# Kernel tuning notes

Hardware: AMD Instinct MI355X
Metric: run time of the kernel (lower is better)

The kernel has to match this reference:

```python
import jax, jax.numpy as jnp
import numpy as np

B = 64        # number of jagged segments
LMAX = 1024   # max_seq_len
D = 512       # input feature dim
K = 512       # output feature dim
NW = 128      # number of selectable weight matrices
T = 32768     # total jagged tokens (avg len 512)


def setup_inputs() -> dict:
    rng = np.random.default_rng(0)
    # Monotone offsets with avg segment length T//B = 512, jittered +/-200
    # so every length stays in (0, LMAX].
    offsets = np.arange(B + 1, dtype=np.int64) * (T // B)
    offsets[1:-1] += rng.integers(-200, 200, size=B - 1)
    key = jax.random.key(0)
    k1, k2, k3, k4 = jax.random.split(key, 4)
    jagged = jax.random.normal(k1, (T, D), dtype=jnp.float32)
    weight = jax.random.normal(k2, (NW, D, K), dtype=jnp.float32) * 0.02
    bias = jax.random.normal(k3, (NW, K), dtype=jnp.float32)
    index = jax.random.randint(k4, (B,), 0, NW)
    return {
        "max_seq_len": LMAX,
        "offsets": jnp.asarray(offsets),
        "index": index,
        "jagged": jagged,
        "weight": weight,
        "bias": bias,
    }


def reference(max_seq_len, offsets, index, jagged, weight, bias):
    # out[offsets[b]:offsets[b+1]] = jagged[offsets[b]:offsets[b+1]] @ weight[index[b]] + bias[index[b]]
    T_, Dd = jagged.shape
    Kk = weight.shape[-1]
    starts = offsets[:-1]            # [B]
    ends = offsets[1:]               # [B]
    pos = starts[:, None] + jnp.arange(max_seq_len)[None, :]   # [B, L] global row ids
    valid = pos < ends[:, None]                                # [B, L]
    safe = jnp.where(valid, pos, 0)
    padded = jnp.where(valid[..., None], jagged[safe], 0)      # [B, L, D]
    w = weight[index]                                          # [B, D, K] (index-select)
    b = bias[index]                                            # [B, K]
    out_p = jnp.einsum("bld,bdk->blk", padded, w) + b[:, None, :]  # [B, L, K]
    # Scatter padded result back to jagged layout; invalid slots go to row T_ (dropped).
    scatter_idx = jnp.where(valid, pos, T_)
    out = jnp.zeros((T_ + 1, Kk), jagged.dtype).at[scatter_idx].set(out_p)
    return out[:T_]
```

## Files before the change

### kernel.cpp

```cpp
#include <hip/hip_runtime.h>
#include <hip/hip_bf16.h>

#define D_DIM 512
#define K_DIM 512
#define B_C   64
#define LMAX_C 1024

#define BM 128
#define BN 128
#define BK 64
#define KSTEPS (D_DIM / BK)
#define ROWT (LMAX_C / BM)
#define COLT (K_DIM / BN)
#define NWG  (B_C * ROWT * COLT)
#define SB 64

typedef __attribute__((ext_vector_type(8))) short bf16x8;
typedef __attribute__((ext_vector_type(4))) short bf16x4;
typedef __attribute__((ext_vector_type(4))) float f32x4;

__device__ __forceinline__ short f2bf(float f) {
    union { __hip_bfloat16 h; short s; } u;
    u.h = __float2bfloat16(f);
    return u.s;
}

__device__ __forceinline__ short* lds_addr(short* base, int row, int kbyte) {
    return (short*)((char*)base + row * 128 + (kbyte ^ ((row & 7) << 4)));
}

__global__ __launch_bounds__(256) void jbmm_kernel(
    const int* __restrict__ offsets,
    const int* __restrict__ index,
    const float* __restrict__ jagged,
    const float* __restrict__ weight,
    const float* __restrict__ bias,
    float* __restrict__ out)
{
    __shared__ short As[BM * SB];
    __shared__ short Bs[BN * SB];

    const int bidRaw = blockIdx.x;
    const int bid = (bidRaw & 7) * (NWG / 8) + (bidRaw >> 3);

    const int b   = bid / (ROWT * COLT);
    const int rt  = (bid / COLT) % ROWT;
    const int ct  = bid % COLT;

    const int start = offsets[b];
    const int end   = offsets[b + 1];
    const int m0    = start + rt * BM;
    if (m0 >= end) return;
    const int rows = (end - m0) < BM ? (end - m0) : BM;

    const int idxw = index[b];
    const float* W = weight + (size_t)idxw * D_DIM * K_DIM;
    const int n0 = ct * BN;

    const int tid  = threadIdx.x;
    const int lane = tid & 63;
    const int wid  = tid >> 6;
    const int wr   = wid >> 1;
    const int wc   = wid & 1;
    const int lr   = lane & 15;
    const int lg   = lane >> 4;

    const int arow  = tid >> 3;
    const int acol8 = tid & 7;
    const int dq = lane >> 2;
    const int nq = lane & 3;

    float bias_v[4];
#pragma unroll
    for (int ni = 0; ni < 4; ++ni)
        bias_v[ni] = bias[(size_t)idxw * K_DIM + n0 + wc * 64 + ni * 16 + lr];

    f32x4 acc[4][4];
#pragma unroll
    for (int mi = 0; mi < 4; ++mi)
#pragma unroll
        for (int ni = 0; ni < 4; ++ni)
            acc[mi][ni] = (f32x4){0.f, 0.f, 0.f, 0.f};

    f32x4 aR[8];
    f32x4 bR[8];

#define LOADA(k0_)                                                          \
    {                                                                       \
        _Pragma("unroll")                                                   \
        for (int i = 0; i < 4; ++i) {                                       \
            const int r = arow + 32 * i;                                    \
            f32x4 v0 = (f32x4){0.f,0.f,0.f,0.f};                            \
            f32x4 v1 = (f32x4){0.f,0.f,0.f,0.f};                            \
            if (r < rows) {                                                 \
                const float* p = &jagged[(size_t)(m0 + r) * D_DIM + (k0_) + acol8 * 8]; \
                v0 = *reinterpret_cast<const f32x4*>(p);                    \
                v1 = *reinterpret_cast<const f32x4*>(p + 4);                \
            }                                                               \
            aR[2 * i] = v0; aR[2 * i + 1] = v1;                             \
        }                                                                   \
    }

#define LOADB(k0_)                                                          \
    {                                                                       \
        _Pragma("unroll")                                                   \
        for (int rep = 0; rep < 2; ++rep) {                                 \
            const int n = n0 + (wid * 2 + rep) * 16 + nq * 4;               \
            _Pragma("unroll")                                               \
            for (int i = 0; i < 4; ++i)                                     \
                bR[rep * 4 + i] = *reinterpret_cast<const f32x4*>(          \
                    &W[(size_t)((k0_) + dq * 4 + i) * K_DIM + n]);          \
        }                                                                   \
    }

#define STORE_LDS()                                                         \
    {                                                                       \
        _Pragma("unroll")                                                   \
        for (int i = 0; i < 4; ++i) {                                       \
            const int r = arow + 32 * i;                                    \
            bf16x8 w;                                                       \
            w[0] = f2bf(aR[2*i][0]); w[1] = f2bf(aR[2*i][1]);               \
            w[2] = f2bf(aR[2*i][2]); w[3] = f2bf(aR[2*i][3]);               \
            w[4] = f2bf(aR[2*i+1][0]); w[5] = f2bf(aR[2*i+1][1]);           \
            w[6] = f2bf(aR[2*i+1][2]); w[7] = f2bf(aR[2*i+1][3]);           \
            *reinterpret_cast<bf16x8*>(lds_addr(As, r, acol8 * 16)) = w;    \
        }                                                                   \
        _Pragma("unroll")                                                   \
        for (int rep = 0; rep < 2; ++rep) {                                 \
            const int nb = (wid * 2 + rep) * 16 + nq * 4;                   \
            _Pragma("unroll")                                               \
            for (int j = 0; j < 4; ++j) {                                   \
                bf16x4 tv;                                                  \
                tv[0] = f2bf(bR[rep*4+0][j]); tv[1] = f2bf(bR[rep*4+1][j]); \
                tv[2] = f2bf(bR[rep*4+2][j]); tv[3] = f2bf(bR[rep*4+3][j]); \
                *reinterpret_cast<bf16x4*>(lds_addr(Bs, nb + j, dq * 8)) = tv; \
            }                                                               \
        }                                                                   \
    }

    LOADA(0); LOADB(0);

    for (int t = 0; t < KSTEPS; ++t) {
        STORE_LDS();
        __syncthreads();
        if (t + 1 < KSTEPS) {
            const int knext = (t + 1) * BK;
            LOADA(knext); LOADB(knext);
        }
#pragma unroll
        for (int kh = 0; kh < 2; ++kh) {
            bf16x8 af[4], bfr[4];
#pragma unroll
            for (int mi = 0; mi < 4; ++mi)
                af[mi] = *reinterpret_cast<bf16x8*>(
                    lds_addr(As, wr * 64 + mi * 16 + lr, kh * 64 + lg * 16));
#pragma unroll
            for (int ni = 0; ni < 4; ++ni)
                bfr[ni] = *reinterpret_cast<bf16x8*>(
                    lds_addr(Bs, wc * 64 + ni * 16 + lr, kh * 64 + lg * 16));
#pragma unroll
            for (int mi = 0; mi < 4; ++mi)
#pragma unroll
                for (int ni = 0; ni < 4; ++ni)
                    acc[mi][ni] = __builtin_amdgcn_mfma_f32_16x16x32_bf16(
                        af[mi], bfr[ni], acc[mi][ni], 0, 0, 0);
        }
        __syncthreads();
    }

#pragma unroll
    for (int mi = 0; mi < 4; ++mi) {
        const int rloc = wr * 64 + mi * 16 + lg * 4;
#pragma unroll
        for (int r = 0; r < 4; ++r) {
            const int rr = rloc + r;
            if (rr < rows) {
#pragma unroll
                for (int ni = 0; ni < 4; ++ni) {
                    out[(size_t)(m0 + rr) * K_DIM + n0 + wc * 64 + ni * 16 + lr] =
                        acc[mi][ni][r] + bias_v[ni];
                }
            }
        }
    }
}

extern "C" void kernel_launch(void* const* d_in, const int* in_sizes, int n_in,
                              void* d_out, int out_size, void* d_ws, size_t ws_size,
                              hipStream_t stream) {
    const int*   offsets = (const int*)d_in[1];
    const int*   index   = (const int*)d_in[2];
    const float* jagged  = (const float*)d_in[3];
    const float* weight  = (const float*)d_in[4];
    const float* bias    = (const float*)d_in[5];
    float*       out     = (float*)d_out;

    dim3 grid(NWG);
    dim3 block(256);
    hipLaunchKernelGGL(jbmm_kernel, grid, block, 0, stream,
                       offsets, index, jagged, weight, bias, out);
}
```

Baseline: 47.88 us.

## Double-buffer LDS tiles with prefetch-two pipeline and wider B stores

Measured after the change: 47.66 us. No clear change (-0.5%).

```diff
diff --git a/kernel.cpp b/kernel.cpp
--- a/kernel.cpp
+++ b/kernel.cpp
@@ -9,14 +9,12 @@
 #define BM 128
 #define BN 128
 #define BK 64
-#define KSTEPS (D_DIM / BK)
-#define ROWT (LMAX_C / BM)
-#define COLT (K_DIM / BN)
+#define KSTEPS 8
+#define ROWT 8
+#define COLT 4
 #define NWG  (B_C * ROWT * COLT)
-#define SB 64
 
 typedef __attribute__((ext_vector_type(8))) short bf16x8;
-typedef __attribute__((ext_vector_type(4))) short bf16x4;
 typedef __attribute__((ext_vector_type(4))) float f32x4;
 
 __device__ __forceinline__ short f2bf(float f) {
@@ -26,10 +24,11 @@
 }
 
 __device__ __forceinline__ short* lds_addr(short* base, int row, int kbyte) {
-    return (short*)((char*)base + row * 128 + (kbyte ^ ((row & 7) << 4)));
-}
-
-__global__ __launch_bounds__(256) void jbmm_kernel(
+    return (short*)((char*)base + row * 128 +
+                    (kbyte ^ ((((row & 7) ^ ((row >> 2) & 7))) << 4)));
+}
+
+__global__ __launch_bounds__(256, 2) void jbmm_kernel(
     const int* __restrict__ offsets,
     const int* __restrict__ index,
     const float* __restrict__ jagged,
@@ -37,8 +36,8 @@
     const float* __restrict__ bias,
     float* __restrict__ out)
 {
-    __shared__ short As[BM * SB];
-    __shared__ short Bs[BN * SB];
+    __shared__ short As[2][BM * BK];
+    __shared__ short Bs[2][BN * BK];
 
     const int bidRaw = blockIdx.x;
     const int bid = (bidRaw & 7) * (NWG / 8) + (bidRaw >> 3);
@@ -67,8 +66,8 @@
 
     const int arow  = tid >> 3;
     const int acol8 = tid & 7;
-    const int dq = lane >> 2;
-    const int nq = lane & 3;
+    const int n4    = tid & 31;
+    const int dq8   = tid >> 5;
 
     float bias_v[4];
 #pragma unroll
@@ -104,16 +103,12 @@
 #define LOADB(k0_)                                                          \
     {                                                                       \
         _Pragma("unroll")                                                   \
-        for (int rep = 0; rep < 2; ++rep) {                                 \
-            const int n = n0 + (wid * 2 + rep) * 16 + nq * 4;               \
-            _Pragma("unroll")                                               \
-            for (int i = 0; i < 4; ++i)                                     \
-                bR[rep * 4 + i] = *reinterpret_cast<const f32x4*>(          \
-                    &W[(size_t)((k0_) + dq * 4 + i) * K_DIM + n]);          \
-        }                                                                   \
-    }
-
-#define STORE_LDS()                                                         \
+        for (int j = 0; j < 8; ++j)                                         \
+            bR[j] = *reinterpret_cast<const f32x4*>(                        \
+                &W[(size_t)((k0_) + dq8 * 8 + j) * K_DIM + n0 + n4 * 4]);   \
+    }
+
+#define CVTSTORE(c_)                                                        \
     {                                                                       \
         _Pragma("unroll")                                                   \
         for (int i = 0; i < 4; ++i) {                                       \
@@ -123,49 +118,57 @@
             w[2] = f2bf(aR[2*i][2]); w[3] = f2bf(aR[2*i][3]);               \
             w[4] = f2bf(aR[2*i+1][0]); w[5] = f2bf(aR[2*i+1][1]);           \
             w[6] = f2bf(aR[2*i+1][2]); w[7] = f2bf(aR[2*i+1][3]);           \
-            *reinterpret_cast<bf16x8*>(lds_addr(As, r, acol8 * 16)) = w;    \
-        }                                                                   \
-        _Pragma("unroll")                                                   \
-        for (int rep = 0; rep < 2; ++rep) {                                 \
-            const int nb = (wid * 2 + rep) * 16 + nq * 4;                   \
+            *reinterpret_cast<bf16x8*>(lds_addr(&As[c_][0], r, acol8 * 16)) = w; \
+        }                                                                   \
+        _Pragma("unroll")                                                   \
+        for (int np = 0; np < 4; ++np) {                                    \
+            bf16x8 w;                                                       \
+            w[0] = f2bf(bR[0][np]); w[1] = f2bf(bR[1][np]);                 \
+            w[2] = f2bf(bR[2][np]); w[3] = f2bf(bR[3][np]);                 \
+            w[4] = f2bf(bR[4][np]); w[5] = f2bf(bR[5][np]);                 \
+            w[6] = f2bf(bR[6][np]); w[7] = f2bf(bR[7][np]);                 \
+            *reinterpret_cast<bf16x8*>(lds_addr(&Bs[c_][0], n4 * 4 + np, dq8 * 16)) = w; \
+        }                                                                   \
+    }
+
+#define COMPUTE(c_)                                                         \
+    {                                                                       \
+        _Pragma("unroll")                                                   \
+        for (int kh = 0; kh < 2; ++kh) {                                    \
+            bf16x8 af[4], bfr[4];                                           \
             _Pragma("unroll")                                               \
-            for (int j = 0; j < 4; ++j) {                                   \
-                bf16x4 tv;                                                  \
-                tv[0] = f2bf(bR[rep*4+0][j]); tv[1] = f2bf(bR[rep*4+1][j]); \
-                tv[2] = f2bf(bR[rep*4+2][j]); tv[3] = f2bf(bR[rep*4+3][j]); \
-                *reinterpret_cast<bf16x4*>(lds_addr(Bs, nb + j, dq * 8)) = tv; \
-            }                                                               \
+            for (int mi = 0; mi < 4; ++mi)                                  \
+                af[mi] = *reinterpret_cast<bf16x8*>(                        \
+                    lds_addr(&As[c_][0], wr * 64 + mi * 16 + lr, kh * 64 + lg * 16)); \
+            _Pragma("unroll")                                               \
+            for (int ni = 0; ni < 4; ++ni)                                  \
+                bfr[ni] = *reinterpret_cast<bf16x8*>(                       \
+                    lds_addr(&Bs[c_][0], wc * 64 + ni * 16 + lr, kh * 64 + lg * 16)); \
+            _Pragma("unroll")                                               \
+            for (int mi = 0; mi < 4; ++mi)                                  \
+                _Pragma("unroll")                                           \
+                for (int ni = 0; ni < 4; ++ni)                              \
+                    acc[mi][ni] = __builtin_amdgcn_mfma_f32_16x16x32_bf16(  \
+                        af[mi], bfr[ni], acc[mi][ni], 0, 0, 0);             \
         }                                                                   \
     }
 
     LOADA(0); LOADB(0);
-
+    CVTSTORE(0);
+    LOADA(BK); LOADB(BK);
+    __syncthreads();
+
+#pragma unroll
     for (int t = 0; t < KSTEPS; ++t) {
-        STORE_LDS();
-        __syncthreads();
+        COMPUTE(t & 1);
         if (t + 1 < KSTEPS) {
-            const int knext = (t + 1) * BK;
-            LOADA(knext); LOADB(knext);
+            CVTSTORE((t + 1) & 1);
+            if (t + 2 < KSTEPS) {
+                const int kn = (t + 2) * BK;
+                LOADA(kn); LOADB(kn);
+            }
+            __syncthreads();
         }
-#pragma unroll
-        for (int kh = 0; kh < 2; ++kh) {
-            bf16x8 af[4], bfr[4];
-#pragma unroll
-            for (int mi = 0; mi < 4; ++mi)
-                af[mi] = *reinterpret_cast<bf16x8*>(
-                    lds_addr(As, wr * 64 + mi * 16 + lr, kh * 64 + lg * 16));
-#pragma unroll
-            for (int ni = 0; ni < 4; ++ni)
-                bfr[ni] = *reinterpret_cast<bf16x8*>(
-                    lds_addr(Bs, wc * 64 + ni * 16 + lr, kh * 64 + lg * 16));
-#pragma unroll
-            for (int mi = 0; mi < 4; ++mi)
-#pragma unroll
-                for (int ni = 0; ni < 4; ++ni)
-                    acc[mi][ni] = __builtin_amdgcn_mfma_f32_16x16x32_bf16(
-                        af[mi], bfr[ni], acc[mi][ni], 0, 0, 0);
-        }
-        __syncthreads();
     }
 
 #pragma unroll
```
